# Kernel tuning notes

Hardware: AMD Instinct MI355X
Metric: run time of the kernel (lower is better)

## Reference

```python
import jax, jax.numpy as jnp
import numpy as np

B, T, IN, H, N, M = 64, 64, 256, 512, 4096, 128
EPS = 1e-8


def setup_inputs() -> dict:
    key = jax.random.key(0)
    ks = jax.random.split(key, 24)
    s = 0.05
    w = lambda k, shape: jax.random.normal(k, shape, jnp.float32) * s
    return {
        "x": jax.random.normal(ks[0], (B, T, 1, IN), jnp.float32),
        "mem0": jax.random.uniform(ks[1], (B, N, M), jnp.float32) * 0.1,
        "Wx": w(ks[2], (IN, H)),
        "Wr": w(ks[3], (M, H)),
        "bC": jnp.zeros((H,), jnp.float32),
        "r_Wk": w(ks[4], (H, M)), "r_bk": jnp.zeros((M,), jnp.float32),
        "r_Wbeta": w(ks[5], (H, 1)), "r_Wg": w(ks[6], (H, 1)),
        "r_Ws": w(ks[7], (H, 3)), "r_Wgam": w(ks[8], (H, 1)),
        "w_Wk": w(ks[9], (H, M)), "w_bk": jnp.zeros((M,), jnp.float32),
        "w_Wbeta": w(ks[10], (H, 1)), "w_Wg": w(ks[11], (H, 1)),
        "w_Ws": w(ks[12], (H, 3)), "w_Wgam": w(ks[13], (H, 1)),
        "w_We": w(ks[14], (H, M)), "w_Wa": w(ks[15], (H, M)),
    }


def _address(h, w_prev, mem, Wk, bk, Wbeta, Wg, Ws, Wgam):
    # h: [B,H], w_prev: [B,N], mem: [B,N,M]
    k = jnp.tanh(h @ Wk + bk)                      # [B,M]
    beta = jax.nn.softplus(h @ Wbeta)              # [B,1]
    g = jax.nn.sigmoid(h @ Wg)                     # [B,1]
    s = jax.nn.softmax(h @ Ws, axis=-1)            # [B,3]
    gamma = 1.0 + jax.nn.softplus(h @ Wgam)        # [B,1]
    # cosine similarity content addressing
    dot = jnp.einsum('bnm,bm->bn', mem, k)         # [B,N]
    mnorm = jnp.linalg.norm(mem, axis=-1)          # [B,N]
    knorm = jnp.linalg.norm(k, axis=-1, keepdims=True)  # [B,1]
    wc = jax.nn.softmax(beta * dot / (mnorm * knorm + EPS), axis=-1)
    wg = g * wc + (1.0 - g) * w_prev               # [B,N]
    # circular shift with 3 taps {-1, 0, +1}
    wt = (s[:, 0:1] * jnp.roll(wg, -1, axis=1)
          + s[:, 1:2] * wg
          + s[:, 2:3] * jnp.roll(wg, 1, axis=1))
    wp = (wt + EPS) ** gamma                        # sharpen
    return wp / jnp.sum(wp, axis=-1, keepdims=True)


def reference(x, mem0, Wx, Wr, bC,
              r_Wk, r_bk, r_Wbeta, r_Wg, r_Ws, r_Wgam,
              w_Wk, w_bk, w_Wbeta, w_Wg, w_Ws, w_Wgam, w_We, w_Wa):
    xt = x.reshape(B, T, -1).transpose(1, 0, 2)    # [T,B,IN]
    w0 = jnp.zeros((B, N), jnp.float32).at[0, 0].set(1.0)
    h0 = jnp.zeros((B, H), jnp.float32)

    def step(carry, x_t):
        mem, wr, ww, h = carry
        # write to memory using previous hidden and ww (erase then add)
        e = jax.nn.sigmoid(h @ w_We)               # [B,M]
        a = jnp.tanh(h @ w_Wa)                     # [B,M]
        mem = mem * (1.0 - ww[:, :, None] * e[:, None, :]) \
              + ww[:, :, None] * a[:, None, :]     # [B,N,M]
        # read
        r = jnp.einsum('bn,bnm->bm', wr, mem)      # [B,M]
        # controller step
        h = jnp.tanh(x_t @ Wx + r @ Wr + bC)       # [B,H]
        # new addressing weights
        wr = _address(h, wr, mem, r_Wk, r_bk, r_Wbeta, r_Wg, r_Ws, r_Wgam)
        ww = _address(h, ww, mem, w_Wk, w_bk, w_Wbeta, w_Wg, w_Ws, w_Wgam)
        return (mem, wr, ww, h), None

    (mem, wr, ww, h), _ = jax.lax.scan(step, (mem0, w0, w0, h0), xt)
    return h                                       # last hidden state [B,H]
```

## Files before the change

kernel.cpp:

```cpp
#include <hip/hip_runtime.h>
#include <hip/hip_bf16.h>
#include <math.h>

#define BB 64
#define TT 64
#define INDIM 256
#define HH 512
#define NN 4096
#define MM 128
#define SS 32
#define ROWS 128
#define EPSF 1e-8f

__device__ __forceinline__ float sigmoidf_(float x){ return 1.f/(1.f+expf(-x)); }
__device__ __forceinline__ float softplusf_(float x){ return (x>20.f)? x : log1pf(expf(x)); }

__device__ __forceinline__ void unpack2(unsigned u, float& lo, float& hi){
  lo = __uint_as_float(u << 16);
  hi = __uint_as_float(u & 0xffff0000u);
}
__device__ __forceinline__ unsigned packrn(float a, float b){
  __hip_bfloat162 p = __float22bfloat162_rn(make_float2(a,b));
  return *reinterpret_cast<unsigned*>(&p);
}

__global__ __launch_bounds__(256) void kCvt(const float* __restrict__ src,
                                            uint4* __restrict__ dst){
  const size_t i = (size_t)blockIdx.x*blockDim.x + threadIdx.x;
  const float4 f0 = *(const float4*)(src + i*8);
  const float4 f1 = *(const float4*)(src + i*8 + 4);
  uint4 q;
  q.x = packrn(f0.x, f0.y); q.y = packrn(f0.z, f0.w);
  q.z = packrn(f1.x, f1.y); q.w = packrn(f1.z, f1.w);
  dst[i] = q;
}

__global__ __launch_bounds__(512) void kPre(const float* __restrict__ x,
                                            const float* __restrict__ Wx,
                                            const float* __restrict__ bC,
                                            float* __restrict__ xwx){
  const int bt = blockIdx.x, t = threadIdx.x;
  __shared__ float xs[INDIM];
  if (t < INDIM) xs[t] = x[(size_t)bt*INDIM + t];
  __syncthreads();
  float acc = bC[t];
  #pragma unroll 4
  for (int i=0;i<INDIM;++i) acc += xs[i]*Wx[(size_t)i*HH + t];
  xwx[(size_t)bt*HH + t] = acc;
}

__global__ __launch_bounds__(256) void kA(
    const float* __restrict__ eG, const float* __restrict__ aG,
    const float* __restrict__ wrG, const float* __restrict__ wwG,
    uint4* __restrict__ mem, float* __restrict__ rpart, float* __restrict__ mnormG)
{
  const int b = blockIdx.y;
  const int n0 = blockIdx.x * ROWS;
  const int t = threadIdx.x;
  const int grp = t >> 4, lane = t & 15;
  const int m0 = lane * 8;
  float ev[8], av[8];
  {
    const float4 e0 = *(const float4*)(eG + b*MM + m0);
    const float4 e1 = *(const float4*)(eG + b*MM + m0 + 4);
    const float4 a0 = *(const float4*)(aG + b*MM + m0);
    const float4 a1 = *(const float4*)(aG + b*MM + m0 + 4);
    ev[0]=e0.x; ev[1]=e0.y; ev[2]=e0.z; ev[3]=e0.w;
    ev[4]=e1.x; ev[5]=e1.y; ev[6]=e1.z; ev[7]=e1.w;
    av[0]=a0.x; av[1]=a0.y; av[2]=a0.z; av[3]=a0.w;
    av[4]=a1.x; av[5]=a1.y; av[6]=a1.z; av[7]=a1.w;
  }
  float wwv[8], wrv[8];
  #pragma unroll
  for (int rr=0; rr<8; ++rr){
    const int n = n0 + rr*16 + grp;
    wwv[rr] = wwG[b*NN+n];
    wrv[rr] = wrG[b*NN+n];
  }
  float racc[8];
  #pragma unroll
  for (int j=0;j<8;++j) racc[j]=0.f;
  __shared__ float lr[16][128];
  const size_t base4 = ((size_t)b*NN + n0)*(MM/8) + (size_t)grp*(MM/8) + lane;
  uint4 q = mem[base4];
  #pragma unroll
  for (int rr=0; rr<8; ++rr){
    uint4 qn;
    if (rr<7) qn = mem[base4 + (size_t)(rr+1)*16*(MM/8)];
    const int n = n0 + rr*16 + grp;
    float v[8];
    unpack2(q.x, v[0], v[1]); unpack2(q.y, v[2], v[3]);
    unpack2(q.z, v[4], v[5]); unpack2(q.w, v[6], v[7]);
    float sq = 0.f;
    const float w = wwv[rr], wr_ = wrv[rr];
    #pragma unroll
    for (int j=0;j<8;++j){
      v[j] = v[j]*(1.f - w*ev[j]) + w*av[j];
      racc[j] += wr_*v[j];
      sq += v[j]*v[j];
    }
    uint4 q2;
    q2.x = packrn(v[0],v[1]); q2.y = packrn(v[2],v[3]);
    q2.z = packrn(v[4],v[5]); q2.w = packrn(v[6],v[7]);
    mem[base4 + (size_t)rr*16*(MM/8)] = q2;
    #pragma unroll
    for (int msk=1; msk<16; msk<<=1) sq += __shfl_xor(sq, msk);
    if (lane==0) mnormG[b*NN+n] = sqrtf(sq);
    q = qn;
  }
  #pragma unroll
  for (int j=0;j<8;++j) lr[grp][m0+j] = racc[j];
  __syncthreads();
  if (t < MM){
    float s=0.f;
    #pragma unroll
    for (int g=0; g<16; ++g) s += lr[g][t];
    rpart[((size_t)b*SS + blockIdx.x)*MM + t] = s;
  }
}

__global__ __launch_bounds__(1024) void kB(
    const float* __restrict__ xwx, int tstep,
    const float* __restrict__ Wr,
    const float* __restrict__ rWk, const float* __restrict__ rbk,
    const float* __restrict__ rWbeta, const float* __restrict__ rWg,
    const float* __restrict__ rWs, const float* __restrict__ rWgam,
    const float* __restrict__ wWk, const float* __restrict__ wbk,
    const float* __restrict__ wWbeta, const float* __restrict__ wWg,
    const float* __restrict__ wWs, const float* __restrict__ wWgam,
    const float* __restrict__ wWe, const float* __restrict__ wWa,
    const float* __restrict__ rpart,
    float* __restrict__ hG, float* __restrict__ krG, float* __restrict__ kwG,
    float* __restrict__ eG, float* __restrict__ aG, float* __restrict__ scal,
    float* __restrict__ outG)
{
  const int b = blockIdx.x, t = threadIdx.x;
  __shared__ float rs[MM], hs[HH], ks[2*MM], sd[14], hd[8][128];
  if (t < MM){
    float s=0.f;
    #pragma unroll
    for (int i=0;i<SS;++i) s += rpart[((size_t)b*SS+i)*MM + t];
    rs[t]=s;
  }
  __syncthreads();
  if (t < HH){
    float acc = xwx[((size_t)b*TT + tstep)*HH + t];
    #pragma unroll 4
    for (int m=0;m<MM;++m) acc += rs[m]*Wr[(size_t)m*HH + t];
    float hv = tanhf(acc);
    hs[t]=hv; hG[(size_t)b*HH+t]=hv;
    if (tstep == TT-1) outG[(size_t)b*HH+t]=hv;
  }
  __syncthreads();
  {
    const int q = t >> 7, m = t & 127;
    const int head = q & 3, jh = q >> 2;
    const float* W = (head==0)? rWk : (head==1)? wWk : (head==2)? wWe : wWa;
    float acc = 0.f;
    const int j0 = jh*256;
    #pragma unroll 4
    for (int j=j0; j<j0+256; ++j) acc += hs[j]*W[(size_t)j*MM + m];
    hd[q][m] = acc;
  }
  __syncthreads();
  if (t < 512){
    const int q = t >> 7, m = t & 127;
    float acc = hd[q][m] + hd[q+4][m];
    if (q==0){ float v=tanhf(acc + rbk[m]); ks[m]=v;    krG[b*MM+m]=v; }
    else if (q==1){ float v=tanhf(acc + wbk[m]); ks[MM+m]=v; kwG[b*MM+m]=v; }
    else if (q==2){ eG[b*MM+m]=sigmoidf_(acc); }
    else          { aG[b*MM+m]=tanhf(acc); }
  }
  __syncthreads();
  {
    const int wv = t>>6, ln = t&63;
    if (wv < 14){
      const int jj = wv;
      float acc=0.f;
      if (jj==6 || jj==13){
        const int o = (jj==6)? 0 : MM;
        const float v1=ks[o+ln], v2=ks[o+64+ln];
        acc = v1*v1 + v2*v2;
      } else {
        const int j2 = (jj<7)? jj : jj-7;
        const bool rd = (jj<7);
        const float* W; int C, c;
        switch (j2){
          case 0: W = rd? rWbeta : wWbeta; C=1; c=0; break;
          case 1: W = rd? rWg   : wWg;    C=1; c=0; break;
          case 2: W = rd? rWgam : wWgam;  C=1; c=0; break;
          default: W = rd? rWs  : wWs;    C=3; c=j2-3; break;
        }
        for (int j=ln; j<HH; j+=64) acc += hs[j]*W[j*C + c];
      }
      #pragma unroll
      for (int msk=1; msk<64; msk<<=1) acc += __shfl_xor(acc, msk);
      if (ln==0) sd[jj]=acc;
    }
  }
  __syncthreads();
  if (t==0){
    float* sc = scal + b*16;
    sc[0] = softplusf_(sd[0]);
    sc[1] = sigmoidf_(sd[1]);
    sc[2] = 1.f + softplusf_(sd[2]);
    {
      float mx = fmaxf(sd[3], fmaxf(sd[4], sd[5]));
      float e0=expf(sd[3]-mx), e1=expf(sd[4]-mx), e2=expf(sd[5]-mx);
      float inv=1.f/(e0+e1+e2);
      sc[3]=e0*inv; sc[4]=e1*inv; sc[5]=e2*inv;
    }
    sc[6] = sqrtf(sd[6]);
    sc[8]  = softplusf_(sd[7]);
    sc[9]  = sigmoidf_(sd[8]);
    sc[10] = 1.f + softplusf_(sd[9]);
    {
      float mx = fmaxf(sd[10], fmaxf(sd[11], sd[12]));
      float e0=expf(sd[10]-mx), e1=expf(sd[11]-mx), e2=expf(sd[12]-mx);
      float inv=1.f/(e0+e1+e2);
      sc[11]=e0*inv; sc[12]=e1*inv; sc[13]=e2*inv;
    }
    sc[14] = sqrtf(sd[13]);
  }
}

__global__ __launch_bounds__(256) void kC(
    const uint4* __restrict__ mem,
    const float* __restrict__ krG, const float* __restrict__ kwG,
    float* __restrict__ dotrG, float* __restrict__ dotwG)
{
  const int b = blockIdx.y;
  const int n0 = blockIdx.x * ROWS;
  const int t = threadIdx.x, grp=t>>4, lane=t&15;
  const int m0 = lane*8;
  float krv[8], kwv[8];
  {
    const float4 k0 = *(const float4*)(krG + b*MM + m0);
    const float4 k1 = *(const float4*)(krG + b*MM + m0 + 4);
    const float4 w0 = *(const float4*)(kwG + b*MM + m0);
    const float4 w1 = *(const float4*)(kwG + b*MM + m0 + 4);
    krv[0]=k0.x; krv[1]=k0.y; krv[2]=k0.z; krv[3]=k0.w;
    krv[4]=k1.x; krv[5]=k1.y; krv[6]=k1.z; krv[7]=k1.w;
    kwv[0]=w0.x; kwv[1]=w0.y; kwv[2]=w0.z; kwv[3]=w0.w;
    kwv[4]=w1.x; kwv[5]=w1.y; kwv[6]=w1.z; kwv[7]=w1.w;
  }
  const size_t base4 = ((size_t)b*NN + n0)*(MM/8) + (size_t)grp*(MM/8) + lane;
  uint4 q = mem[base4];
  #pragma unroll
  for (int rr=0; rr<8; ++rr){
    uint4 qn;
    if (rr<7) qn = mem[base4 + (size_t)(rr+1)*16*(MM/8)];
    const int n = n0 + rr*16 + grp;
    float v[8];
    unpack2(q.x, v[0], v[1]); unpack2(q.y, v[2], v[3]);
    unpack2(q.z, v[4], v[5]); unpack2(q.w, v[6], v[7]);
    float dr=0.f, dw=0.f;
    #pragma unroll
    for (int j=0;j<8;++j){ dr += v[j]*krv[j]; dw += v[j]*kwv[j]; }
    #pragma unroll
    for (int msk=1; msk<16; msk<<=1){
      dr += __shfl_xor(dr, msk);
      dw += __shfl_xor(dw, msk);
    }
    if (lane==0){ dotrG[b*NN+n]=dr; dotwG[b*NN+n]=dw; }
    q = qn;
  }
}

__device__ __forceinline__ float blockSum256(float v, volatile float* sc){
  #pragma unroll
  for (int m=1;m<64;m<<=1) v += __shfl_xor(v,m);
  __syncthreads();
  if ((threadIdx.x&63)==0) sc[threadIdx.x>>6]=v;
  __syncthreads();
  return sc[0]+sc[1]+sc[2]+sc[3];
}
__device__ __forceinline__ float blockMax256(float v, volatile float* sc){
  #pragma unroll
  for (int m=1;m<64;m<<=1) v = fmaxf(v, __shfl_xor(v,m));
  __syncthreads();
  if ((threadIdx.x&63)==0) sc[threadIdx.x>>6]=v;
  __syncthreads();
  return fmaxf(fmaxf(sc[0],sc[1]), fmaxf(sc[2],sc[3]));
}

__global__ __launch_bounds__(256) void kD(
    const float* __restrict__ dotrG, const float* __restrict__ dotwG,
    const float* __restrict__ mnormG, const float* __restrict__ scal,
    float* __restrict__ wrG, float* __restrict__ wwG)
{
  const int b = blockIdx.x, head = blockIdx.y, t = threadIdx.x;
  __shared__ float wg[NN];
  __shared__ float sc[4];
  const float* dot = head? dotwG : dotrG;
  float* wv = head? wwG : wrG;
  const float* sb = scal + b*16 + head*8;
  const float beta=sb[0], g=sb[1], gamma=sb[2];
  const float s0=sb[3], s1=sb[4], s2=sb[5], knorm=sb[6];
  float sim[16]; float mx = -1e30f;
  #pragma unroll
  for (int i=0;i<16;++i){
    const int n = i*256 + t;
    const float d  = dot[(size_t)b*NN+n];
    const float mn = mnormG[(size_t)b*NN+n];
    sim[i] = beta*d/(mn*knorm + EPSF);
    mx = fmaxf(mx, sim[i]);
  }
  mx = blockMax256(mx, sc);
  float sum=0.f;
  #pragma unroll
  for (int i=0;i<16;++i){ sim[i]=__expf(sim[i]-mx); sum += sim[i]; }
  sum = blockSum256(sum, sc);
  const float inv = 1.f/sum;
  #pragma unroll
  for (int i=0;i<16;++i){
    const int n = i*256 + t;
    wg[n] = g*sim[i]*inv + (1.f-g)*wv[(size_t)b*NN+n];
  }
  __syncthreads();
  float wp[16]; float ps=0.f;
  #pragma unroll
  for (int i=0;i<16;++i){
    const int n = i*256 + t;
    const float wt = s0*wg[(n+1)&(NN-1)] + s1*wg[n] + s2*wg[(n-1)&(NN-1)];
    wp[i] = __powf(wt + EPSF, gamma);
    ps += wp[i];
  }
  ps = blockSum256(ps, sc);
  const float ip = 1.f/ps;
  #pragma unroll
  for (int i=0;i<16;++i){
    const int n = i*256 + t;
    wv[(size_t)b*NN+n] = wp[i]*ip;
  }
}

__global__ void kInit(float* wr, float* ww, float* h, float* e, float* a){
  const int i = blockIdx.x*blockDim.x + threadIdx.x;
  if (i < BB*NN){ const float v = (i==0)? 1.f : 0.f; wr[i]=v; ww[i]=v; }
  if (i < BB*HH) h[i]=0.f;
  if (i < BB*MM){ e[i]=0.5f; a[i]=0.f; }
}

extern "C" void kernel_launch(void* const* d_in, const int* in_sizes, int n_in,
                              void* d_out, int out_size, void* d_ws, size_t ws_size,
                              hipStream_t stream)
{
  const float* x     = (const float*)d_in[0];
  const float* mem0  = (const float*)d_in[1];
  const float* Wx    = (const float*)d_in[2];
  const float* Wr    = (const float*)d_in[3];
  const float* bC    = (const float*)d_in[4];
  const float* rWk   = (const float*)d_in[5];
  const float* rbk   = (const float*)d_in[6];
  const float* rWbeta= (const float*)d_in[7];
  const float* rWg   = (const float*)d_in[8];
  const float* rWs   = (const float*)d_in[9];
  const float* rWgam = (const float*)d_in[10];
  const float* wWk   = (const float*)d_in[11];
  const float* wbk   = (const float*)d_in[12];
  const float* wWbeta= (const float*)d_in[13];
  const float* wWg   = (const float*)d_in[14];
  const float* wWs   = (const float*)d_in[15];
  const float* wWgam = (const float*)d_in[16];
  const float* wWe   = (const float*)d_in[17];
  const float* wWa   = (const float*)d_in[18];

  float* ws = (float*)d_ws;
  size_t o = 0;
  uint4* mem   = (uint4*)(ws + o); o += (size_t)BB*NN*MM/2;
  float* wr    = ws + o; o += (size_t)BB*NN;
  float* ww    = ws + o; o += (size_t)BB*NN;
  float* h     = ws + o; o += (size_t)BB*HH;
  float* rpart = ws + o; o += (size_t)BB*SS*MM;
  float* e     = ws + o; o += (size_t)BB*MM;
  float* a     = ws + o; o += (size_t)BB*MM;
  float* kr    = ws + o; o += (size_t)BB*MM;
  float* kw    = ws + o; o += (size_t)BB*MM;
  float* mnorm = ws + o; o += (size_t)BB*NN;
  float* dotr  = ws + o; o += (size_t)BB*NN;
  float* dotw  = ws + o; o += (size_t)BB*NN;
  float* scal  = ws + o; o += (size_t)BB*16;
  float* xwx   = ws + o; o += (size_t)BB*TT*HH;

  kCvt<<<(BB*NN*MM/8)/256, 256, 0, stream>>>(mem0, mem);
  kInit<<<(BB*NN+255)/256, 256, 0, stream>>>(wr, ww, h, e, a);
  kPre<<<BB*TT, 512, 0, stream>>>(x, Wx, bC, xwx);

  for (int t=0; t<TT; ++t){
    kA<<<dim3(SS,BB), 256, 0, stream>>>(e, a, wr, ww, mem, rpart, mnorm);
    kB<<<BB, 1024, 0, stream>>>(xwx, t, Wr,
                               rWk, rbk, rWbeta, rWg, rWs, rWgam,
                               wWk, wbk, wWbeta, wWg, wWs, wWgam, wWe, wWa,
                               rpart, h, kr, kw, e, a, scal, (float*)d_out);
    if (t < TT-1){
      kC<<<dim3(SS,BB), 256, 0, stream>>>(mem, kr, kw, dotr, dotw);
      kD<<<dim3(BB,2), 256, 0, stream>>>(dotr, dotw, mnorm, scal, wr, ww);
    }
  }
}
```

Before: 5.054 ms.

## Fuse controller, content-dot and addressing kernels into one per-batch kernel

```diff
diff --git a/kernel.cpp b/kernel.cpp
--- a/kernel.cpp
+++ b/kernel.cpp
@@ -119,7 +119,30 @@
   }
 }
 
-__global__ __launch_bounds__(1024) void kB(
+__device__ __forceinline__ float bmax1024(float v, volatile float* red){
+  #pragma unroll
+  for (int m=1;m<64;m<<=1) v = fmaxf(v, __shfl_xor(v,m));
+  __syncthreads();
+  if ((threadIdx.x&63)==0) red[threadIdx.x>>6]=v;
+  __syncthreads();
+  float s=red[0];
+  #pragma unroll
+  for (int g=1;g<16;++g) s = fmaxf(s, red[g]);
+  return s;
+}
+__device__ __forceinline__ float bsum1024(float v, volatile float* red){
+  #pragma unroll
+  for (int m=1;m<64;m<<=1) v += __shfl_xor(v,m);
+  __syncthreads();
+  if ((threadIdx.x&63)==0) red[threadIdx.x>>6]=v;
+  __syncthreads();
+  float s=0.f;
+  #pragma unroll
+  for (int g=0;g<16;++g) s += red[g];
+  return s;
+}
+
+__global__ __launch_bounds__(1024) void kBCD(
     const float* __restrict__ xwx, int tstep,
     const float* __restrict__ Wr,
     const float* __restrict__ rWk, const float* __restrict__ rbk,
@@ -130,12 +153,16 @@
     const float* __restrict__ wWs, const float* __restrict__ wWgam,
     const float* __restrict__ wWe, const float* __restrict__ wWa,
     const float* __restrict__ rpart,
-    float* __restrict__ hG, float* __restrict__ krG, float* __restrict__ kwG,
-    float* __restrict__ eG, float* __restrict__ aG, float* __restrict__ scal,
+    const uint4* __restrict__ mem, const float* __restrict__ mnormG,
+    float* __restrict__ eG, float* __restrict__ aG,
+    float* __restrict__ wrG, float* __restrict__ wwG,
     float* __restrict__ outG)
 {
   const int b = blockIdx.x, t = threadIdx.x;
-  __shared__ float rs[MM], hs[HH], ks[2*MM], sd[14], hd[8][128];
+  __shared__ float rs[MM], hs[HH], ks[2*MM], sd[14], hd[8][128], sc2[16];
+  __shared__ float drS[NN], dwS[NN], wgS[NN];
+  __shared__ float red[16];
+
   if (t < MM){
     float s=0.f;
     #pragma unroll
@@ -148,10 +175,11 @@
     #pragma unroll 4
     for (int m=0;m<MM;++m) acc += rs[m]*Wr[(size_t)m*HH + t];
     float hv = tanhf(acc);
-    hs[t]=hv; hG[(size_t)b*HH+t]=hv;
+    hs[t]=hv;
     if (tstep == TT-1) outG[(size_t)b*HH+t]=hv;
   }
   __syncthreads();
+  if (tstep == TT-1) return;
   {
     const int q = t >> 7, m = t & 127;
     const int head = q & 3, jh = q >> 2;
@@ -166,8 +194,8 @@
   if (t < 512){
     const int q = t >> 7, m = t & 127;
     float acc = hd[q][m] + hd[q+4][m];
-    if (q==0){ float v=tanhf(acc + rbk[m]); ks[m]=v;    krG[b*MM+m]=v; }
-    else if (q==1){ float v=tanhf(acc + wbk[m]); ks[MM+m]=v; kwG[b*MM+m]=v; }
+    if (q==0){ ks[m]    = tanhf(acc + rbk[m]); }
+    else if (q==1){ ks[MM+m] = tanhf(acc + wbk[m]); }
     else if (q==2){ eG[b*MM+m]=sigmoidf_(acc); }
     else          { aG[b*MM+m]=tanhf(acc); }
   }
@@ -200,145 +228,103 @@
   }
   __syncthreads();
   if (t==0){
-    float* sc = scal + b*16;
-    sc[0] = softplusf_(sd[0]);
-    sc[1] = sigmoidf_(sd[1]);
-    sc[2] = 1.f + softplusf_(sd[2]);
+    sc2[0] = softplusf_(sd[0]);
+    sc2[1] = sigmoidf_(sd[1]);
+    sc2[2] = 1.f + softplusf_(sd[2]);
     {
       float mx = fmaxf(sd[3], fmaxf(sd[4], sd[5]));
       float e0=expf(sd[3]-mx), e1=expf(sd[4]-mx), e2=expf(sd[5]-mx);
       float inv=1.f/(e0+e1+e2);
-      sc[3]=e0*inv; sc[4]=e1*inv; sc[5]=e2*inv;
-    }
-    sc[6] = sqrtf(sd[6]);
-    sc[8]  = softplusf_(sd[7]);
-    sc[9]  = sigmoidf_(sd[8]);
-    sc[10] = 1.f + softplusf_(sd[9]);
+      sc2[3]=e0*inv; sc2[4]=e1*inv; sc2[5]=e2*inv;
+    }
+    sc2[6] = sqrtf(sd[6]);
+    sc2[8]  = softplusf_(sd[7]);
+    sc2[9]  = sigmoidf_(sd[8]);
+    sc2[10] = 1.f + softplusf_(sd[9]);
     {
       float mx = fmaxf(sd[10], fmaxf(sd[11], sd[12]));
       float e0=expf(sd[10]-mx), e1=expf(sd[11]-mx), e2=expf(sd[12]-mx);
       float inv=1.f/(e0+e1+e2);
-      sc[11]=e0*inv; sc[12]=e1*inv; sc[13]=e2*inv;
-    }
-    sc[14] = sqrtf(sd[13]);
-  }
-}
-
-__global__ __launch_bounds__(256) void kC(
-    const uint4* __restrict__ mem,
-    const float* __restrict__ krG, const float* __restrict__ kwG,
-    float* __restrict__ dotrG, float* __restrict__ dotwG)
-{
-  const int b = blockIdx.y;
-  const int n0 = blockIdx.x * ROWS;
-  const int t = threadIdx.x, grp=t>>4, lane=t&15;
-  const int m0 = lane*8;
-  float krv[8], kwv[8];
+      sc2[11]=e0*inv; sc2[12]=e1*inv; sc2[13]=e2*inv;
+    }
+    sc2[14] = sqrtf(sd[13]);
+  }
+  __syncthreads();
   {
-    const float4 k0 = *(const float4*)(krG + b*MM + m0);
-    const float4 k1 = *(const float4*)(krG + b*MM + m0 + 4);
-    const float4 w0 = *(const float4*)(kwG + b*MM + m0);
-    const float4 w1 = *(const float4*)(kwG + b*MM + m0 + 4);
-    krv[0]=k0.x; krv[1]=k0.y; krv[2]=k0.z; krv[3]=k0.w;
-    krv[4]=k1.x; krv[5]=k1.y; krv[6]=k1.z; krv[7]=k1.w;
-    kwv[0]=w0.x; kwv[1]=w0.y; kwv[2]=w0.z; kwv[3]=w0.w;
-    kwv[4]=w1.x; kwv[5]=w1.y; kwv[6]=w1.z; kwv[7]=w1.w;
-  }
-  const size_t base4 = ((size_t)b*NN + n0)*(MM/8) + (size_t)grp*(MM/8) + lane;
-  uint4 q = mem[base4];
-  #pragma unroll
-  for (int rr=0; rr<8; ++rr){
-    uint4 qn;
-    if (rr<7) qn = mem[base4 + (size_t)(rr+1)*16*(MM/8)];
-    const int n = n0 + rr*16 + grp;
-    float v[8];
-    unpack2(q.x, v[0], v[1]); unpack2(q.y, v[2], v[3]);
-    unpack2(q.z, v[4], v[5]); unpack2(q.w, v[6], v[7]);
-    float dr=0.f, dw=0.f;
-    #pragma unroll
-    for (int j=0;j<8;++j){ dr += v[j]*krv[j]; dw += v[j]*kwv[j]; }
-    #pragma unroll
-    for (int msk=1; msk<16; msk<<=1){
-      dr += __shfl_xor(dr, msk);
-      dw += __shfl_xor(dw, msk);
-    }
-    if (lane==0){ dotrG[b*NN+n]=dr; dotwG[b*NN+n]=dw; }
-    q = qn;
-  }
-}
-
-__device__ __forceinline__ float blockSum256(float v, volatile float* sc){
-  #pragma unroll
-  for (int m=1;m<64;m<<=1) v += __shfl_xor(v,m);
-  __syncthreads();
-  if ((threadIdx.x&63)==0) sc[threadIdx.x>>6]=v;
-  __syncthreads();
-  return sc[0]+sc[1]+sc[2]+sc[3];
-}
-__device__ __forceinline__ float blockMax256(float v, volatile float* sc){
-  #pragma unroll
-  for (int m=1;m<64;m<<=1) v = fmaxf(v, __shfl_xor(v,m));
-  __syncthreads();
-  if ((threadIdx.x&63)==0) sc[threadIdx.x>>6]=v;
-  __syncthreads();
-  return fmaxf(fmaxf(sc[0],sc[1]), fmaxf(sc[2],sc[3]));
-}
-
-__global__ __launch_bounds__(256) void kD(
-    const float* __restrict__ dotrG, const float* __restrict__ dotwG,
-    const float* __restrict__ mnormG, const float* __restrict__ scal,
-    float* __restrict__ wrG, float* __restrict__ wwG)
-{
-  const int b = blockIdx.x, head = blockIdx.y, t = threadIdx.x;
-  __shared__ float wg[NN];
-  __shared__ float sc[4];
-  const float* dot = head? dotwG : dotrG;
-  float* wv = head? wwG : wrG;
-  const float* sb = scal + b*16 + head*8;
-  const float beta=sb[0], g=sb[1], gamma=sb[2];
-  const float s0=sb[3], s1=sb[4], s2=sb[5], knorm=sb[6];
-  float sim[16]; float mx = -1e30f;
-  #pragma unroll
-  for (int i=0;i<16;++i){
-    const int n = i*256 + t;
-    const float d  = dot[(size_t)b*NN+n];
-    const float mn = mnormG[(size_t)b*NN+n];
-    sim[i] = beta*d/(mn*knorm + EPSF);
-    mx = fmaxf(mx, sim[i]);
-  }
-  mx = blockMax256(mx, sc);
-  float sum=0.f;
-  #pragma unroll
-  for (int i=0;i<16;++i){ sim[i]=__expf(sim[i]-mx); sum += sim[i]; }
-  sum = blockSum256(sum, sc);
-  const float inv = 1.f/sum;
-  #pragma unroll
-  for (int i=0;i<16;++i){
-    const int n = i*256 + t;
-    wg[n] = g*sim[i]*inv + (1.f-g)*wv[(size_t)b*NN+n];
-  }
-  __syncthreads();
-  float wp[16]; float ps=0.f;
-  #pragma unroll
-  for (int i=0;i<16;++i){
-    const int n = i*256 + t;
-    const float wt = s0*wg[(n+1)&(NN-1)] + s1*wg[n] + s2*wg[(n-1)&(NN-1)];
-    wp[i] = __powf(wt + EPSF, gamma);
-    ps += wp[i];
-  }
-  ps = blockSum256(ps, sc);
-  const float ip = 1.f/ps;
-  #pragma unroll
-  for (int i=0;i<16;++i){
-    const int n = i*256 + t;
-    wv[(size_t)b*NN+n] = wp[i]*ip;
-  }
-}
-
-__global__ void kInit(float* wr, float* ww, float* h, float* e, float* a){
+    const int grp = t >> 4, lane = t & 15;
+    const int m0 = lane*8;
+    float krv[8], kwv[8];
+    #pragma unroll
+    for (int j=0;j<8;++j){ krv[j]=ks[m0+j]; kwv[j]=ks[MM+m0+j]; }
+    const size_t base4 = ((size_t)b*NN)*(MM/8) + (size_t)grp*(MM/8) + lane;
+    uint4 q = mem[base4];
+    for (int rr=0; rr<64; ++rr){
+      uint4 qn;
+      if (rr<63) qn = mem[base4 + (size_t)(rr+1)*64*(MM/8)];
+      const int n = rr*64 + grp;
+      float v[8];
+      unpack2(q.x, v[0], v[1]); unpack2(q.y, v[2], v[3]);
+      unpack2(q.z, v[4], v[5]); unpack2(q.w, v[6], v[7]);
+      float dr=0.f, dw=0.f;
+      #pragma unroll
+      for (int j=0;j<8;++j){ dr += v[j]*krv[j]; dw += v[j]*kwv[j]; }
+      #pragma unroll
+      for (int msk=1; msk<16; msk<<=1){
+        dr += __shfl_xor(dr, msk);
+        dw += __shfl_xor(dw, msk);
+      }
+      if (lane==0){ drS[n]=dr; dwS[n]=dw; }
+      q = qn;
+    }
+  }
+  __syncthreads();
+  for (int head=0; head<2; ++head){
+    const float* dotL = head? dwS : drS;
+    float* wv = head? wwG : wrG;
+    const float* sb = sc2 + head*8;
+    const float beta=sb[0], g=sb[1], gamma=sb[2];
+    const float s0=sb[3], s1=sb[4], s2=sb[5], knorm=sb[6];
+    float sim[4]; float mx = -1e30f;
+    #pragma unroll
+    for (int i=0;i<4;++i){
+      const int n = i*1024 + t;
+      sim[i] = beta*dotL[n]/(mnormG[(size_t)b*NN+n]*knorm + EPSF);
+      mx = fmaxf(mx, sim[i]);
+    }
+    mx = bmax1024(mx, red);
+    float sum=0.f;
+    #pragma unroll
+    for (int i=0;i<4;++i){ sim[i]=__expf(sim[i]-mx); sum += sim[i]; }
+    sum = bsum1024(sum, red);
+    const float inv = 1.f/sum;
+    #pragma unroll
+    for (int i=0;i<4;++i){
+      const int n = i*1024 + t;
+      wgS[n] = g*sim[i]*inv + (1.f-g)*wv[(size_t)b*NN+n];
+    }
+    __syncthreads();
+    float wp[4]; float ps=0.f;
+    #pragma unroll
+    for (int i=0;i<4;++i){
+      const int n = i*1024 + t;
+      const float wt = s0*wgS[(n+1)&(NN-1)] + s1*wgS[n] + s2*wgS[(n-1)&(NN-1)];
+      wp[i] = __powf(wt + EPSF, gamma);
+      ps += wp[i];
+    }
+    ps = bsum1024(ps, red);
+    const float ip = 1.f/ps;
+    #pragma unroll
+    for (int i=0;i<4;++i){
+      const int n = i*1024 + t;
+      wv[(size_t)b*NN+n] = wp[i]*ip;
+    }
+    __syncthreads();
+  }
+}
+
+__global__ void kInit(float* wr, float* ww, float* e, float* a){
   const int i = blockIdx.x*blockDim.x + threadIdx.x;
   if (i < BB*NN){ const float v = (i==0)? 1.f : 0.f; wr[i]=v; ww[i]=v; }
-  if (i < BB*HH) h[i]=0.f;
   if (i < BB*MM){ e[i]=0.5f; a[i]=0.f; }
 }
 
@@ -371,31 +357,21 @@
   uint4* mem   = (uint4*)(ws + o); o += (size_t)BB*NN*MM/2;
   float* wr    = ws + o; o += (size_t)BB*NN;
   float* ww    = ws + o; o += (size_t)BB*NN;
-  float* h     = ws + o; o += (size_t)BB*HH;
   float* rpart = ws + o; o += (size_t)BB*SS*MM;
   float* e     = ws + o; o += (size_t)BB*MM;
   float* a     = ws + o; o += (size_t)BB*MM;
-  float* kr    = ws + o; o += (size_t)BB*MM;
-  float* kw    = ws + o; o += (size_t)BB*MM;
   float* mnorm = ws + o; o += (size_t)BB*NN;
-  float* dotr  = ws + o; o += (size_t)BB*NN;
-  float* dotw  = ws + o; o += (size_t)BB*NN;
-  float* scal  = ws + o; o += (size_t)BB*16;
   float* xwx   = ws + o; o += (size_t)BB*TT*HH;
 
   kCvt<<<(BB*NN*MM/8)/256, 256, 0, stream>>>(mem0, mem);
-  kInit<<<(BB*NN+255)/256, 256, 0, stream>>>(wr, ww, h, e, a);
+  kInit<<<(BB*NN+255)/256, 256, 0, stream>>>(wr, ww, e, a);
   kPre<<<BB*TT, 512, 0, stream>>>(x, Wx, bC, xwx);
 
   for (int t=0; t<TT; ++t){
     kA<<<dim3(SS,BB), 256, 0, stream>>>(e, a, wr, ww, mem, rpart, mnorm);
-    kB<<<BB, 1024, 0, stream>>>(xwx, t, Wr,
+    kBCD<<<BB, 1024, 0, stream>>>(xwx, t, Wr,
                                rWk, rbk, rWbeta, rWg, rWs, rWgam,
                                wWk, wbk, wWbeta, wWg, wWs, wWgam, wWe, wWa,
-                               rpart, h, kr, kw, e, a, scal, (float*)d_out);
-    if (t < TT-1){
-      kC<<<dim3(SS,BB), 256, 0, stream>>>(mem, kr, kw, dotr, dotw);
-      kD<<<dim3(BB,2), 256, 0, stream>>>(dotr, dotw, mnorm, scal, wr, ww);
-    }
-  }
-}
+                               rpart, mem, mnorm, e, a, wr, ww, (float*)d_out);
+  }
+}
```

Result: slower. 6.434 ms (+27.3%).

## Split controller kernel into batched tiled GEMMs with packed head weights

Applied to the files above, without the earlier changes.

```diff
diff --git a/kernel.cpp b/kernel.cpp
--- a/kernel.cpp
+++ b/kernel.cpp
@@ -10,9 +10,11 @@
 #define MM 128
 #define SS 32
 #define ROWS 128
+#define WC 544
 #define EPSF 1e-8f
 
-__device__ __forceinline__ float sigmoidf_(float x){ return 1.f/(1.f+expf(-x)); }
+__device__ __forceinline__ float fsig(float x){ return 1.f/(1.f+__expf(-x)); }
+__device__ __forceinline__ float ftanh(float x){ return 1.f - 2.f/(__expf(2.f*x)+1.f); }
 __device__ __forceinline__ float softplusf_(float x){ return (x>20.f)? x : log1pf(expf(x)); }
 
 __device__ __forceinline__ void unpack2(unsigned u, float& lo, float& hi){
@@ -35,22 +37,76 @@
   dst[i] = q;
 }
 
+__global__ void kInit(float* wr, float* ww, float* headout){
+  const int i = blockIdx.x*blockDim.x + threadIdx.x;
+  if (i < BB*NN){ const float v = (i==0)? 1.f : 0.f; wr[i]=v; ww[i]=v; }
+  if (i < BB*WC) headout[i]=0.f;
+}
+
+__global__ __launch_bounds__(576) void kPack(
+    const float* __restrict__ rWk, const float* __restrict__ wWk,
+    const float* __restrict__ wWe, const float* __restrict__ wWa,
+    const float* __restrict__ rWbeta, const float* __restrict__ rWg,
+    const float* __restrict__ rWs, const float* __restrict__ rWgam,
+    const float* __restrict__ wWbeta, const float* __restrict__ wWg,
+    const float* __restrict__ wWs, const float* __restrict__ wWgam,
+    float* __restrict__ Wall)
+{
+  const int j = blockIdx.x, c = threadIdx.x;
+  if (c >= WC) return;
+  float v = 0.f;
+  if      (c < 128) v = rWk[(size_t)j*128 + c];
+  else if (c < 256) v = wWk[(size_t)j*128 + c-128];
+  else if (c < 384) v = wWe[(size_t)j*128 + c-256];
+  else if (c < 512) v = wWa[(size_t)j*128 + c-384];
+  else {
+    const int cc = c - 512;
+    switch (cc){
+      case 0:  v = rWbeta[j]; break;
+      case 1:  v = rWg[j];    break;
+      case 2: case 3: case 4: v = rWs[(size_t)j*3 + cc-2]; break;
+      case 5:  v = rWgam[j];  break;
+      case 6:  v = wWbeta[j]; break;
+      case 7:  v = wWg[j];    break;
+      case 8: case 9: case 10: v = wWs[(size_t)j*3 + cc-8]; break;
+      case 11: v = wWgam[j];  break;
+      default: v = 0.f; break;
+    }
+  }
+  Wall[(size_t)j*WC + c] = v;
+}
+
 __global__ __launch_bounds__(512) void kPre(const float* __restrict__ x,
                                             const float* __restrict__ Wx,
                                             const float* __restrict__ bC,
                                             float* __restrict__ xwx){
-  const int bt = blockIdx.x, t = threadIdx.x;
-  __shared__ float xs[INDIM];
-  if (t < INDIM) xs[t] = x[(size_t)bt*INDIM + t];
-  __syncthreads();
-  float acc = bC[t];
-  #pragma unroll 4
-  for (int i=0;i<INDIM;++i) acc += xs[i]*Wx[(size_t)i*HH + t];
-  xwx[(size_t)bt*HH + t] = acc;
+  const int bt0 = blockIdx.x*16, t = threadIdx.x;
+  __shared__ float xs[INDIM][16];
+  for (int lin = t; lin < 16*INDIM; lin += 512){
+    const int ii = lin & 255, r = lin >> 8;
+    xs[ii][r] = x[(size_t)(bt0+r)*INDIM + ii];
+  }
+  __syncthreads();
+  float accv[16];
+  #pragma unroll
+  for (int r=0;r<16;++r) accv[r]=0.f;
+  for (int ii=0; ii<INDIM; ++ii){
+    const float w = Wx[(size_t)ii*HH + t];
+    const float4* xp = (const float4*)&xs[ii][0];
+    const float4 x0=xp[0], x1=xp[1], x2=xp[2], x3=xp[3];
+    accv[0]+=x0.x*w; accv[1]+=x0.y*w; accv[2]+=x0.z*w; accv[3]+=x0.w*w;
+    accv[4]+=x1.x*w; accv[5]+=x1.y*w; accv[6]+=x1.z*w; accv[7]+=x1.w*w;
+    accv[8]+=x2.x*w; accv[9]+=x2.y*w; accv[10]+=x2.z*w; accv[11]+=x2.w*w;
+    accv[12]+=x3.x*w; accv[13]+=x3.y*w; accv[14]+=x3.z*w; accv[15]+=x3.w*w;
+  }
+  const float bc = bC[t];
+  #pragma unroll
+  for (int r=0;r<16;++r)
+    xwx[(size_t)(bt0+r)*HH + t] = accv[r] + bc;
 }
 
 __global__ __launch_bounds__(256) void kA(
-    const float* __restrict__ eG, const float* __restrict__ aG,
+    const float* __restrict__ headout,
     const float* __restrict__ wrG, const float* __restrict__ wwG,
     uint4* __restrict__ mem, float* __restrict__ rpart, float* __restrict__ mnormG)
 {
@@ -59,16 +115,12 @@
   const int t = threadIdx.x;
   const int grp = t >> 4, lane = t & 15;
   const int m0 = lane * 8;
+  const float* HO = headout + (size_t)b*WC;
   float ev[8], av[8];
-  {
-    const float4 e0 = *(const float4*)(eG + b*MM + m0);
-    const float4 e1 = *(const float4*)(eG + b*MM + m0 + 4);
-    const float4 a0 = *(const float4*)(aG + b*MM + m0);
-    const float4 a1 = *(const float4*)(aG + b*MM + m0 + 4);
-    ev[0]=e0.x; ev[1]=e0.y; ev[2]=e0.z; ev[3]=e0.w;
-    ev[4]=e1.x; ev[5]=e1.y; ev[6]=e1.z; ev[7]=e1.w;
-    av[0]=a0.x; av[1]=a0.y; av[2]=a0.z; av[3]=a0.w;
-    av[4]=a1.x; av[5]=a1.y; av[6]=a1.z; av[7]=a1.w;
+  #pragma unroll
+  for (int j=0;j<8;++j){
+    ev[j] = fsig (HO[256 + m0 + j]);
+    av[j] = ftanh(HO[384 + m0 + j]);
   }
   float wwv[8], wrv[8];
   #pragma unroll
@@ -119,130 +171,77 @@
   }
 }
 
-__global__ __launch_bounds__(1024) void kB(
+__global__ __launch_bounds__(256) void kH(
     const float* __restrict__ xwx, int tstep,
-    const float* __restrict__ Wr,
-    const float* __restrict__ rWk, const float* __restrict__ rbk,
-    const float* __restrict__ rWbeta, const float* __restrict__ rWg,
-    const float* __restrict__ rWs, const float* __restrict__ rWgam,
-    const float* __restrict__ wWk, const float* __restrict__ wbk,
-    const float* __restrict__ wWbeta, const float* __restrict__ wWg,
-    const float* __restrict__ wWs, const float* __restrict__ wWgam,
-    const float* __restrict__ wWe, const float* __restrict__ wWa,
-    const float* __restrict__ rpart,
-    float* __restrict__ hG, float* __restrict__ krG, float* __restrict__ kwG,
-    float* __restrict__ eG, float* __restrict__ aG, float* __restrict__ scal,
-    float* __restrict__ outG)
-{
-  const int b = blockIdx.x, t = threadIdx.x;
-  __shared__ float rs[MM], hs[HH], ks[2*MM], sd[14], hd[8][128];
-  if (t < MM){
-    float s=0.f;
-    #pragma unroll
-    for (int i=0;i<SS;++i) s += rpart[((size_t)b*SS+i)*MM + t];
-    rs[t]=s;
-  }
-  __syncthreads();
-  if (t < HH){
-    float acc = xwx[((size_t)b*TT + tstep)*HH + t];
-    #pragma unroll 4
-    for (int m=0;m<MM;++m) acc += rs[m]*Wr[(size_t)m*HH + t];
-    float hv = tanhf(acc);
-    hs[t]=hv; hG[(size_t)b*HH+t]=hv;
-    if (tstep == TT-1) outG[(size_t)b*HH+t]=hv;
-  }
-  __syncthreads();
-  {
-    const int q = t >> 7, m = t & 127;
-    const int head = q & 3, jh = q >> 2;
-    const float* W = (head==0)? rWk : (head==1)? wWk : (head==2)? wWe : wWa;
-    float acc = 0.f;
-    const int j0 = jh*256;
-    #pragma unroll 4
-    for (int j=j0; j<j0+256; ++j) acc += hs[j]*W[(size_t)j*MM + m];
-    hd[q][m] = acc;
-  }
-  __syncthreads();
-  if (t < 512){
-    const int q = t >> 7, m = t & 127;
-    float acc = hd[q][m] + hd[q+4][m];
-    if (q==0){ float v=tanhf(acc + rbk[m]); ks[m]=v;    krG[b*MM+m]=v; }
-    else if (q==1){ float v=tanhf(acc + wbk[m]); ks[MM+m]=v; kwG[b*MM+m]=v; }
-    else if (q==2){ eG[b*MM+m]=sigmoidf_(acc); }
-    else          { aG[b*MM+m]=tanhf(acc); }
-  }
-  __syncthreads();
-  {
-    const int wv = t>>6, ln = t&63;
-    if (wv < 14){
-      const int jj = wv;
-      float acc=0.f;
-      if (jj==6 || jj==13){
-        const int o = (jj==6)? 0 : MM;
-        const float v1=ks[o+ln], v2=ks[o+64+ln];
-        acc = v1*v1 + v2*v2;
-      } else {
-        const int j2 = (jj<7)? jj : jj-7;
-        const bool rd = (jj<7);
-        const float* W; int C, c;
-        switch (j2){
-          case 0: W = rd? rWbeta : wWbeta; C=1; c=0; break;
-          case 1: W = rd? rWg   : wWg;    C=1; c=0; break;
-          case 2: W = rd? rWgam : wWgam;  C=1; c=0; break;
-          default: W = rd? rWs  : wWs;    C=3; c=j2-3; break;
-        }
-        for (int j=ln; j<HH; j+=64) acc += hs[j]*W[j*C + c];
-      }
-      #pragma unroll
-      for (int msk=1; msk<64; msk<<=1) acc += __shfl_xor(acc, msk);
-      if (ln==0) sd[jj]=acc;
+    const float* __restrict__ Wr, const float* __restrict__ rpart,
+    float* __restrict__ hG, float* __restrict__ outG)
+{
+  const int c0 = blockIdx.x*32, b0 = blockIdx.y*8;
+  const int tid = threadIdx.x;
+  const int bb = tid>>5, cc = tid&31;
+  __shared__ float rsS[8][128];
+  __shared__ float WrS[128][32];
+  for (int lin = tid; lin < 8*128; lin += 256){
+    const int rb = lin>>7, m = lin&127;
+    float s = 0.f;
+    #pragma unroll
+    for (int ss=0; ss<SS; ++ss)
+      s += rpart[((size_t)(b0+rb)*SS + ss)*MM + m];
+    rsS[rb][m] = s;
+  }
+  for (int lin = tid; lin < 128*32; lin += 256){
+    const int m = lin>>5, c = lin&31;
+    WrS[m][c] = Wr[(size_t)m*HH + c0 + c];
+  }
+  __syncthreads();
+  float acc = xwx[((size_t)(b0+bb)*TT + tstep)*HH + c0 + cc];
+  #pragma unroll 8
+  for (int m=0;m<128;++m) acc += rsS[bb][m]*WrS[m][cc];
+  const float hv = ftanh(acc);
+  hG[(size_t)(b0+bb)*HH + c0 + cc] = hv;
+  if (tstep == TT-1) outG[(size_t)(b0+bb)*HH + c0 + cc] = hv;
+}
+
+__global__ __launch_bounds__(256) void kB2(
+    const float* __restrict__ hG, const float* __restrict__ Wall,
+    float* __restrict__ headout)
+{
+  const int c0 = blockIdx.x*32, b0 = blockIdx.y*8;
+  const int tid = threadIdx.x;
+  const int bb = tid>>5, cc = tid&31;
+  __shared__ float hs[8][HH];
+  __shared__ float WsS[64][32];
+  for (int lin = tid; lin < 8*HH; lin += 256)
+    hs[lin>>9][lin&511] = hG[(size_t)(b0+(lin>>9))*HH + (lin&511)];
+  float acc = 0.f;
+  for (int ks=0; ks<8; ++ks){
+    __syncthreads();
+    for (int lin = tid; lin < 64*32; lin += 256){
+      const int m = lin>>5, c = lin&31;
+      WsS[m][c] = Wall[(size_t)(ks*64+m)*WC + c0 + c];
     }
-  }
-  __syncthreads();
-  if (t==0){
-    float* sc = scal + b*16;
-    sc[0] = softplusf_(sd[0]);
-    sc[1] = sigmoidf_(sd[1]);
-    sc[2] = 1.f + softplusf_(sd[2]);
-    {
-      float mx = fmaxf(sd[3], fmaxf(sd[4], sd[5]));
-      float e0=expf(sd[3]-mx), e1=expf(sd[4]-mx), e2=expf(sd[5]-mx);
-      float inv=1.f/(e0+e1+e2);
-      sc[3]=e0*inv; sc[4]=e1*inv; sc[5]=e2*inv;
-    }
-    sc[6] = sqrtf(sd[6]);
-    sc[8]  = softplusf_(sd[7]);
-    sc[9]  = sigmoidf_(sd[8]);
-    sc[10] = 1.f + softplusf_(sd[9]);
-    {
-      float mx = fmaxf(sd[10], fmaxf(sd[11], sd[12]));
-      float e0=expf(sd[10]-mx), e1=expf(sd[11]-mx), e2=expf(sd[12]-mx);
-      float inv=1.f/(e0+e1+e2);
-      sc[11]=e0*inv; sc[12]=e1*inv; sc[13]=e2*inv;
-    }
-    sc[14] = sqrtf(sd[13]);
-  }
+    __syncthreads();
+    #pragma unroll 8
+    for (int m=0;m<64;++m) acc += hs[bb][ks*64+m]*WsS[m][cc];
+  }
+  headout[(size_t)(b0+bb)*WC + c0 + cc] = acc;
 }
 
 __global__ __launch_bounds__(256) void kC(
-    const uint4* __restrict__ mem,
-    const float* __restrict__ krG, const float* __restrict__ kwG,
+    const uint4* __restrict__ mem, const float* __restrict__ headout,
+    const float* __restrict__ rbk, const float* __restrict__ wbk,
     float* __restrict__ dotrG, float* __restrict__ dotwG)
 {
   const int b = blockIdx.y;
   const int n0 = blockIdx.x * ROWS;
   const int t = threadIdx.x, grp=t>>4, lane=t&15;
   const int m0 = lane*8;
+  const float* HO = headout + (size_t)b*WC;
   float krv[8], kwv[8];
-  {
-    const float4 k0 = *(const float4*)(krG + b*MM + m0);
-    const float4 k1 = *(const float4*)(krG + b*MM + m0 + 4);
-    const float4 w0 = *(const float4*)(kwG + b*MM + m0);
-    const float4 w1 = *(const float4*)(kwG + b*MM + m0 + 4);
-    krv[0]=k0.x; krv[1]=k0.y; krv[2]=k0.z; krv[3]=k0.w;
-    krv[4]=k1.x; krv[5]=k1.y; krv[6]=k1.z; krv[7]=k1.w;
-    kwv[0]=w0.x; kwv[1]=w0.y; kwv[2]=w0.z; kwv[3]=w0.w;
-    kwv[4]=w1.x; kwv[5]=w1.y; kwv[6]=w1.z; kwv[7]=w1.w;
+  #pragma unroll
+  for (int j=0;j<8;++j){
+    krv[j] = ftanh(HO[m0+j]     + rbk[m0+j]);
+    kwv[j] = ftanh(HO[128+m0+j] + wbk[m0+j]);
   }
   const size_t base4 = ((size_t)b*NN + n0)*(MM/8) + (size_t)grp*(MM/8) + lane;
   uint4 q = mem[base4];
@@ -286,15 +285,40 @@
 
 __global__ __launch_bounds__(256) void kD(
     const float* __restrict__ dotrG, const float* __restrict__ dotwG,
-    const float* __restrict__ mnormG, const float* __restrict__ scal,
+    const float* __restrict__ mnormG, const float* __restrict__ headout,
+    const float* __restrict__ rbk, const float* __restrict__ wbk,
     float* __restrict__ wrG, float* __restrict__ wwG)
 {
   const int b = blockIdx.x, head = blockIdx.y, t = threadIdx.x;
   __shared__ float wg[NN];
   __shared__ float sc[4];
+  __shared__ float sb[8];
+  __shared__ float kred[2];
+  const float* HO = headout + (size_t)b*WC;
+  const float* bk = head? wbk : rbk;
+  if (t < 128){
+    const float km = ftanh(HO[head*128 + t] + bk[t]);
+    float s = km*km;
+    #pragma unroll
+    for (int m=1;m<64;m<<=1) s += __shfl_xor(s, m);
+    if ((t&63)==0) kred[t>>6]=s;
+  }
+  __syncthreads();
+  if (t==0){
+    const int sbase = 512 + head*6;
+    sb[0] = softplusf_(HO[sbase+0]);
+    sb[1] = fsig(HO[sbase+1]);
+    sb[2] = 1.f + softplusf_(HO[sbase+5]);
+    const float s0=HO[sbase+2], s1=HO[sbase+3], s2=HO[sbase+4];
+    const float mx = fmaxf(s0, fmaxf(s1,s2));
+    const float e0=__expf(s0-mx), e1=__expf(s1-mx), e2=__expf(s2-mx);
+    const float inv=1.f/(e0+e1+e2);
+    sb[3]=e0*inv; sb[4]=e1*inv; sb[5]=e2*inv;
+    sb[6] = sqrtf(kred[0]+kred[1]);
+  }
+  __syncthreads();
   const float* dot = head? dotwG : dotrG;
   float* wv = head? wwG : wrG;
-  const float* sb = scal + b*16 + head*8;
   const float beta=sb[0], g=sb[1], gamma=sb[2];
   const float s0=sb[3], s1=sb[4], s2=sb[5], knorm=sb[6];
   float sim[16]; float mx = -1e30f;
@@ -333,13 +357,6 @@
     const int n = i*256 + t;
     wv[(size_t)b*NN+n] = wp[i]*ip;
   }
-}
-
-__global__ void kInit(float* wr, float* ww, float* h, float* e, float* a){
-  const int i = blockIdx.x*blockDim.x + threadIdx.x;
-  if (i < BB*NN){ const float v = (i==0)? 1.f : 0.f; wr[i]=v; ww[i]=v; }
-  if (i < BB*HH) h[i]=0.f;
-  if (i < BB*MM){ e[i]=0.5f; a[i]=0.f; }
 }
 
 extern "C" void kernel_launch(void* const* d_in, const int* in_sizes, int n_in,
@@ -368,34 +385,33 @@
 
   float* ws = (float*)d_ws;
   size_t o = 0;
-  uint4* mem   = (uint4*)(ws + o); o += (size_t)BB*NN*MM/2;
-  float* wr    = ws + o; o += (size_t)BB*NN;
-  float* ww    = ws + o; o += (size_t)BB*NN;
-  float* h     = ws + o; o += (size_t)BB*HH;
-  float* rpart = ws + o; o += (size_t)BB*SS*MM;
-  float* e     = ws + o; o += (size_t)BB*MM;
-  float* a     = ws + o; o += (size_t)BB*MM;
-  float* kr    = ws + o; o += (size_t)BB*MM;
-  float* kw    = ws + o; o += (size_t)BB*MM;
-  float* mnorm = ws + o; o += (size_t)BB*NN;
-  float* dotr  = ws + o; o += (size_t)BB*NN;
-  float* dotw  = ws + o; o += (size_t)BB*NN;
-  float* scal  = ws + o; o += (size_t)BB*16;
-  float* xwx   = ws + o; o += (size_t)BB*TT*HH;
+  uint4* mem    = (uint4*)(ws + o); o += (size_t)BB*NN*MM/2;
+  float* wr     = ws + o; o += (size_t)BB*NN;
+  float* ww     = ws + o; o += (size_t)BB*NN;
+  float* rpart  = ws + o; o += (size_t)BB*SS*MM;
+  float* mnorm  = ws + o; o += (size_t)BB*NN;
+  float* dotr   = ws + o; o += (size_t)BB*NN;
+  float* dotw   = ws + o; o += (size_t)BB*NN;
+  float* xwx    = ws + o; o += (size_t)BB*TT*HH;
+  float* hG     = ws + o; o += (size_t)BB*HH;
+  float* headout= ws + o; o += (size_t)BB*WC;
+  float* Wall   = ws + o; o += (size_t)HH*WC;
 
   kCvt<<<(BB*NN*MM/8)/256, 256, 0, stream>>>(mem0, mem);
-  kInit<<<(BB*NN+255)/256, 256, 0, stream>>>(wr, ww, h, e, a);
-  kPre<<<BB*TT, 512, 0, stream>>>(x, Wx, bC, xwx);
+  kInit<<<(BB*NN+255)/256, 256, 0, stream>>>(wr, ww, headout);
+  kPack<<<HH, 576, 0, stream>>>(rWk, wWk, wWe, wWa,
+                                rWbeta, rWg, rWs, rWgam,
+                                wWbeta, wWg, wWs, wWgam, Wall);
+  kPre<<<(BB*TT)/16, 512, 0, stream>>>(x, Wx, bC, xwx);
 
   for (int t=0; t<TT; ++t){
-    kA<<<dim3(SS,BB), 256, 0, stream>>>(e, a, wr, ww, mem, rpart, mnorm);
-    kB<<<BB, 1024, 0, stream>>>(xwx, t, Wr,
-                               rWk, rbk, rWbeta, rWg, rWs, rWgam,
-                               wWk, wbk, wWbeta, wWg, wWs, wWgam, wWe, wWa,
-                               rpart, h, kr, kw, e, a, scal, (float*)d_out);
+    kA<<<dim3(SS,BB), 256, 0, stream>>>(headout, wr, ww, mem, rpart, mnorm);
+    kH<<<dim3(16,8), 256, 0, stream>>>(xwx, t, Wr, rpart, hG, (float*)d_out);
     if (t < TT-1){
-      kC<<<dim3(SS,BB), 256, 0, stream>>>(mem, kr, kw, dotr, dotw);
-      kD<<<dim3(BB,2), 256, 0, stream>>>(dotr, dotw, mnorm, scal, wr, ww);
+      kB2<<<dim3(17,8), 256, 0, stream>>>(hG, Wall, headout);
+      kC<<<dim3(SS,BB), 256, 0, stream>>>(mem, headout, rbk, wbk, dotr, dotw);
+      kD<<<dim3(BB,2), 256, 0, stream>>>(dotr, dotw, mnorm, headout,
+                                         rbk, wbk, wr, ww);
     }
   }
 }
```

Result: faster. 4.785 ms (-5.3%).
